# Performance work log

Measured on AMD Instinct MI355X. Metric: run time of the kernel, lower is better.

The kernel has to match this reference:

```python
import jax, jax.numpy as jnp
import numpy as np

N = 20000      # nodes
IN = 256       # in_dim
OUT = 128      # out_dim
S = 8          # num_sect
K = S + 1      # sectors + self branch
EP = 40000     # edges per sector


def setup_inputs() -> dict:
    key = jax.random.key(0)
    ks = jax.random.split(key, 10)
    x = jax.random.normal(ks[0], (N, IN), jnp.float32)
    rows = jax.random.randint(ks[1], (S, EP), 0, N)  # src (adj row)
    cols = jax.random.randint(ks[2], (S, EP), 0, N)  # dst (adj col)
    # degree norms (buffers derived from the graph, as in compute_norm)
    out_deg = np.bincount(np.asarray(rows).ravel(), minlength=N).astype(np.float32)
    in_deg = np.bincount(np.asarray(cols).ravel(), minlength=N).astype(np.float32)
    out_norm = jnp.asarray(np.clip(out_deg, 1.0, None) ** -0.5)[:, None]  # [N,1]
    in_norm = jnp.asarray(np.clip(in_deg, 1.0, None) ** -0.5)[:, None]    # [N,1]
    s = 0.05  # xavier-ish scale
    W_self = jax.random.normal(ks[3], (IN, OUT), jnp.float32) * s
    W_sect = jax.random.normal(ks[4], (S, IN, OUT), jnp.float32) * s
    WC = jax.random.normal(ks[5], (OUT, OUT), jnp.float32) * s
    WD = jax.random.normal(ks[6], (OUT, OUT), jnp.float32) * s
    gate_w = jax.random.normal(ks[7], (2 * K * OUT, 1), jnp.float32) * s
    gate_b = jnp.zeros((1,), jnp.float32)
    return {"x": x, "W_self": W_self, "W_sect": W_sect, "WC": WC, "WD": WD,
            "gate_w": gate_w, "gate_b": gate_b, "out_norm": out_norm,
            "in_norm": in_norm, "rows": rows, "cols": cols}


def reference(x, W_self, W_sect, WC, WD, gate_w, gate_b, out_norm, in_norm, rows, cols):
    n = x.shape[0]
    # --- forward_sector_agg (dropout is identity in eval / drop_rate=0) ---
    z_self = x @ W_self                                    # [N, OUT]
    H = jnp.einsum('ni,sio->sno', x, W_sect) * out_norm    # [S, N, OUT]
    def agg(h, r, c):  # sparse adj @ h : z[src] += h[dst]
        return jax.ops.segment_sum(h[c], r, num_segments=n)
    Z = jax.vmap(agg)(H, rows, cols)                       # [S, N, OUT]
    z = jnp.concatenate([z_self[None], Z], axis=0)         # [K, N, OUT]
    z = jnp.transpose(z, (1, 0, 2)) * in_norm[:, :, None]  # [N, K, OUT]
    # --- heter_sen_interaction ---
    zc = z @ WC                                            # [N, K, D]
    com = jnp.einsum('nkd,njd->nkj', zc, zc)
    ac = jax.nn.softmax(com, axis=2)
    z_com = jnp.einsum('nkj,njd->nkd', ac, zc).reshape(n, -1)
    zd = z @ WD
    sub = zd[:, :, None, :] - zd[:, None, :, :]            # [N, K, K, D]
    ds = jnp.einsum('nkd,nkjd->nkj', zd, sub)
    ad = jax.nn.softmax(ds, axis=2)
    z_dis = jnp.einsum('nkj,nkjd->nkd', ad, sub).reshape(n, -1)
    cat = jnp.concatenate([z_com, z_dis], axis=-1)         # [N, 2*K*D]
    beta = jax.nn.sigmoid(cat @ gate_w + gate_b)           # [N, 1]
    return beta * z_com + (1.0 - beta) * z_dis             # [N, K*D]
```

## Files before the change

### kernel.cpp

```cpp
#include <hip/hip_runtime.h>
#include <math.h>

#define N_NODES 20000
#define IN_DIM  256
#define OUT_DIM 128
#define S_SECT  8
#define K_BR    9
#define NK      (K_BR*OUT_DIM)
#define EP_EDGE 40000
#define N_EDGES (S_SECT*EP_EDGE)
#define N_BINS  (S_SECT*N_NODES)
#define SCAN_BLOCKS 160
#define M_ROWS  (N_NODES*K_BR)
#define ZP      136
#define TP      136

typedef float v4f __attribute__((ext_vector_type(4)));
typedef short v8s __attribute__((ext_vector_type(8)));

__device__ inline unsigned short f2bf(float f) {
  union { float f; unsigned u; } v; v.f = f;
  unsigned r = v.u + 0x7fff + ((v.u >> 16) & 1);
  return (unsigned short)(r >> 16);
}
__device__ inline float bf2f(unsigned short h) {
  union { unsigned u; float f; } v; v.u = ((unsigned)h) << 16;
  return v.f;
}

__global__ __launch_bounds__(256) void k_prep(
    const float* __restrict__ Wself, const float* __restrict__ Wsect,
    const float* __restrict__ WC, const float* __restrict__ WD,
    unsigned short* __restrict__ Wtg, unsigned short* __restrict__ Btg)
{
  const int id = blockIdx.x * 256 + threadIdx.x;
  if (id < NK*IN_DIM) {
    const int j = id >> 8, k = id & 255;
    float w;
    if (j < OUT_DIM) w = Wself[(size_t)k*OUT_DIM + j];
    else {
      const int s = (j - OUT_DIM) >> 7, c = (j - OUT_DIM) & 127;
      w = Wsect[(size_t)s*(IN_DIM*OUT_DIM) + (size_t)k*OUT_DIM + c];
    }
    Wtg[id] = f2bf(w);
  } else {
    const int id2 = id - NK*IN_DIM;
    if (id2 < 256*128) {
      const int n = id2 >> 7, k = id2 & 127;
      const float w = (n < OUT_DIM) ? WC[k*OUT_DIM + n] : WD[k*OUT_DIM + (n - OUT_DIM)];
      Btg[id2] = f2bf(w);
    }
  }
}

__global__ __launch_bounds__(256, 4) void k_gemm_xw_mfma(
    const float* __restrict__ x, const unsigned short* __restrict__ Wtg,
    const float* __restrict__ outn, const float* __restrict__ inn,
    unsigned short* __restrict__ Hbuf, unsigned short* __restrict__ Zbufh)
{
  __shared__ unsigned short Bls[128*ZP];
  const int t = threadIdx.x;
  const int wave = t >> 6, lane = t & 63;
  const int mrow = lane & 15, quad = lane >> 4;
  const int m0 = blockIdx.x * 64 + wave * 16;

  v8s afr[8];
  {
    const int r = m0 + mrow;
    const bool ok = (r < N_NODES);
    const float* src = x + (size_t)r*IN_DIM + quad*8;
    #pragma unroll
    for (int kq = 0; kq < 8; ++kq) {
      float4 a0 = {0.f,0.f,0.f,0.f}, a1 = {0.f,0.f,0.f,0.f};
      if (ok) {
        a0 = *(const float4*)(src + kq*32);
        a1 = *(const float4*)(src + kq*32 + 4);
      }
      v8s f;
      f[0] = (short)f2bf(a0.x); f[1] = (short)f2bf(a0.y);
      f[2] = (short)f2bf(a0.z); f[3] = (short)f2bf(a0.w);
      f[4] = (short)f2bf(a1.x); f[5] = (short)f2bf(a1.y);
      f[6] = (short)f2bf(a1.z); f[7] = (short)f2bf(a1.w);
      afr[kq] = f;
    }
  }

  for (int jj = 0; jj < 3; ++jj) {
    const int jb = blockIdx.y * 3 + jj;

    v4f acc[8];
    #pragma unroll
    for (int jt = 0; jt < 8; ++jt) acc[jt] = (v4f){0.f,0.f,0.f,0.f};

    for (int kh = 0; kh < 2; ++kh) {
      #pragma unroll
      for (int i = 0; i < 8; ++i) {
        const int idx = t + i*256;
        const int row = idx >> 4, c8 = idx & 15;
        *(uint4*)(Bls + row*ZP + c8*8) =
            *(const uint4*)(Wtg + (size_t)(jb*128 + row)*IN_DIM + kh*128 + c8*8);
      }
      __syncthreads();

      #pragma unroll
      for (int kq = 0; kq < 4; ++kq) {
        #pragma unroll
        for (int jt = 0; jt < 8; ++jt) {
          const v8s bf = *(const v8s*)(Bls + (jt*16 + mrow)*ZP + kq*32 + quad*8);
          acc[jt] = __builtin_amdgcn_mfma_f32_16x16x32_bf16(afr[kh*4 + kq], bf, acc[jt], 0, 0, 0);
        }
      }
      __syncthreads();
    }

    if (jb == 0) {
      #pragma unroll
      for (int p = 0; p < 4; ++p) {
        const int R = m0 + quad*4 + p;
        if (R >= N_NODES) continue;
        const float iw = inn[R];
        #pragma unroll
        for (int jt = 0; jt < 8; ++jt)
          Zbufh[(size_t)R*NK + jt*16 + mrow] = f2bf(acc[jt][p] * iw);
      }
    } else {
      const int s = jb - 1;
      #pragma unroll
      for (int p = 0; p < 4; ++p) {
        const int R = m0 + quad*4 + p;
        if (R >= N_NODES) continue;
        const float ow = outn[R];
        #pragma unroll
        for (int jt = 0; jt < 8; ++jt)
          Hbuf[((size_t)s*N_NODES + R)*OUT_DIM + jt*16 + mrow] = f2bf(acc[jt][p] * ow);
      }
    }
  }
}

__global__ __launch_bounds__(256) void k_count(
    const int* __restrict__ rows, int* __restrict__ cnt)
{
  const int id = blockIdx.x * 256 + threadIdx.x;
  if (id >= N_EDGES) return;
  const int s = id / EP_EDGE;
  atomicAdd(&cnt[s * N_NODES + rows[id]], 1);
}

__global__ __launch_bounds__(256) void k_scan1(
    const int* __restrict__ cnt, int* __restrict__ bsum)
{
  __shared__ int sh[256];
  const int t = threadIdx.x;
  const int base = blockIdx.x * 1000;
  int s = 0;
  if (t < 250) {
    const int i = base + t*4;
    s = cnt[i] + cnt[i+1] + cnt[i+2] + cnt[i+3];
  }
  sh[t] = s; __syncthreads();
  for (int off = 128; off > 0; off >>= 1) {
    if (t < off) sh[t] += sh[t + off];
    __syncthreads();
  }
  if (t == 0) bsum[blockIdx.x] = sh[0];
}

__global__ void k_scan2(const int* __restrict__ bsum, int* __restrict__ boff)
{
  if (threadIdx.x == 0) {
    int acc = 0;
    for (int b = 0; b < SCAN_BLOCKS; ++b) { boff[b] = acc; acc += bsum[b]; }
  }
}

__global__ __launch_bounds__(256) void k_scan3(
    const int* __restrict__ cnt, const int* __restrict__ boff,
    int* __restrict__ offs)
{
  __shared__ int sh[256];
  const int t = threadIdx.x;
  const int base = blockIdx.x * 1000;
  int v[4] = {0,0,0,0};
  int mySum = 0;
  if (t < 250) {
    const int i = base + t*4;
    v[0]=cnt[i]; v[1]=cnt[i+1]; v[2]=cnt[i+2]; v[3]=cnt[i+3];
    mySum = v[0]+v[1]+v[2]+v[3];
  }
  sh[t] = mySum; __syncthreads();
  for (int off = 1; off < 256; off <<= 1) {
    int add = (t >= off) ? sh[t - off] : 0;
    __syncthreads();
    sh[t] += add;
    __syncthreads();
  }
  if (t < 250) {
    int excl = boff[blockIdx.x] + sh[t] - mySum;
    const int i = base + t*4;
    offs[i]   = excl;           excl += v[0];
    offs[i+1] = excl;           excl += v[1];
    offs[i+2] = excl;           excl += v[2];
    offs[i+3] = excl;
  }
}

__global__ __launch_bounds__(256) void k_scatter(
    const int* __restrict__ rows, const int* __restrict__ cols,
    const int* __restrict__ offs, int* __restrict__ cur,
    int* __restrict__ eCol)
{
  const int id = blockIdx.x * 256 + threadIdx.x;
  if (id >= N_EDGES) return;
  const int s = id / EP_EDGE;
  const int bin = s * N_NODES + rows[id];
  const int pos = offs[bin] + atomicAdd(&cur[bin], 1);
  eCol[pos] = cols[id];
}

__global__ __launch_bounds__(256) void k_agg_csr(
    const unsigned short* __restrict__ Hbuf, const int* __restrict__ offs,
    const int* __restrict__ cnt, const int* __restrict__ eCol,
    const float* __restrict__ inn, unsigned short* __restrict__ Zbufh)
{
  const long long tid = (long long)blockIdx.x * 256 + threadIdx.x;
  const int group = (int)(tid >> 5);
  if (group >= N_BINS) return;
  const int lane = (int)(tid & 31);
  const int s = group / N_NODES;
  const int r = group - s * N_NODES;
  const int start = offs[group];
  const int n = cnt[group];
  float4 acc = {0.f, 0.f, 0.f, 0.f};
  for (int i = 0; i < n; ++i) {
    const int c = eCol[start + i];
    const uint2 h = *(const uint2*)(Hbuf + ((size_t)s*N_NODES + c)*OUT_DIM + lane*4);
    acc.x += bf2f((unsigned short)h.x);
    acc.y += bf2f((unsigned short)(h.x >> 16));
    acc.z += bf2f((unsigned short)h.y);
    acc.w += bf2f((unsigned short)(h.y >> 16));
  }
  const float w = inn[r];
  uint2 o;
  o.x = (unsigned)f2bf(acc.x * w) | ((unsigned)f2bf(acc.y * w) << 16);
  o.y = (unsigned)f2bf(acc.z * w) | ((unsigned)f2bf(acc.w * w) << 16);
  *(uint2*)(Zbufh + ((size_t)r*K_BR + 1 + s)*OUT_DIM + lane*4) = o;
}

__global__ __launch_bounds__(256, 4) void k_gemm_zcd(
    const unsigned short* __restrict__ Zbufh, const unsigned short* __restrict__ Btg,
    unsigned short* __restrict__ ZCD)
{
  __shared__ unsigned short Bls[128*ZP];
  const int t = threadIdx.x;
  const int wave = t >> 6, lane = t & 63;
  const int m0 = blockIdx.x * 128 + wave * 32;
  const int mrow = lane & 15, quad = lane >> 4;

  v8s afr[2][4];
  #pragma unroll
  for (int rb = 0; rb < 2; ++rb) {
    const int r = m0 + rb*16 + mrow;
    const bool ok = (r < M_ROWS);
    const unsigned short* src = Zbufh + (size_t)r*OUT_DIM + quad*8;
    #pragma unroll
    for (int kq = 0; kq < 4; ++kq) {
      v8s f = {0,0,0,0,0,0,0,0};
      if (ok) f = *(const v8s*)(src + kq*32);
      afr[rb][kq] = f;
    }
  }

  for (int jh = 0; jh < 2; ++jh) {
    #pragma unroll
    for (int i = 0; i < 8; ++i) {
      const int idx = t + i*256;
      const int row = idx >> 4, c8 = idx & 15;
      *(uint4*)(Bls + row*ZP + c8*8) =
          *(const uint4*)(Btg + (size_t)(jh*128 + row)*OUT_DIM + c8*8);
    }
    __syncthreads();

    v4f acc[2][8];
    #pragma unroll
    for (int rb = 0; rb < 2; ++rb)
      #pragma unroll
      for (int j = 0; j < 8; ++j) acc[rb][j] = (v4f){0.f,0.f,0.f,0.f};

    #pragma unroll
    for (int j = 0; j < 8; ++j) {
      const unsigned short* bp = Bls + (j*16 + mrow)*ZP + quad*8;
      #pragma unroll
      for (int kq = 0; kq < 4; ++kq) {
        const v8s bf = *(const v8s*)(bp + kq*32);
        acc[0][j] = __builtin_amdgcn_mfma_f32_16x16x32_bf16(afr[0][kq], bf, acc[0][j], 0, 0, 0);
        acc[1][j] = __builtin_amdgcn_mfma_f32_16x16x32_bf16(afr[1][kq], bf, acc[1][j], 0, 0, 0);
      }
    }

    unsigned short* Z = ZCD + (size_t)jh * N_NODES * NK;
    #pragma unroll
    for (int rb = 0; rb < 2; ++rb)
      #pragma unroll
      for (int p = 0; p < 4; ++p) {
        const int R = m0 + rb*16 + quad*4 + p;
        if (R >= M_ROWS) continue;
        const int node = R / 9, kk = R - node*9;
        const size_t base = (size_t)node*NK + kk*OUT_DIM;
        #pragma unroll
        for (int j = 0; j < 8; ++j)
          Z[base + j*16 + mrow] = f2bf(acc[rb][j][p]);
      }
    __syncthreads();
  }
}

__global__ __launch_bounds__(256) void k_interact5(
    const unsigned short* __restrict__ ZCD,
    const float* __restrict__ gw, const float* __restrict__ gb,
    float* __restrict__ out)
{
  __shared__ unsigned short tls[8][2][9*TP];
  __shared__ float graw[8][2][K_BR][10];
  __shared__ float gs[8][2][K_BR][10];
  const int t  = threadIdx.x;
  const int wv = t >> 6, lane = t & 63;
  const int n0 = blockIdx.x * 8;

  {
    const int r = lane & 15, quad = lane >> 4;
    #pragma unroll
    for (int q = 0; q < 4; ++q) {
      const int node = wv*2 + (q >> 1), mat = q & 1;
      const unsigned short* src = ZCD + (size_t)mat*N_NODES*NK
                                  + (size_t)(n0+node)*NK + (size_t)r*OUT_DIM + quad*8;
      v8s frag[4];
      #pragma unroll
      for (int kq = 0; kq < 4; ++kq) {
        v8s f = {0,0,0,0,0,0,0,0};
        if (r < K_BR) f = *(const v8s*)(src + kq*32);
        frag[kq] = f;
      }
      if (r < K_BR) {
        #pragma unroll
        for (int kq = 0; kq < 4; ++kq)
          *(v8s*)&tls[node][mat][r*TP + kq*32 + quad*8] = frag[kq];
      }
      v4f acc = {0.f,0.f,0.f,0.f};
      #pragma unroll
      for (int kq = 0; kq < 4; ++kq)
        acc = __builtin_amdgcn_mfma_f32_16x16x32_bf16(frag[kq], frag[kq], acc, 0, 0, 0);
      if (r < K_BR) {
        #pragma unroll
        for (int p = 0; p < 4; ++p) {
          const int m = quad*4 + p;
          if (m < K_BR) graw[node][mat][m][r] = acc[p];
        }
      }
    }
  }
  __syncthreads();

  if (lane < 36) {
    const int nn2  = (lane >= 18) ? 1 : 0;
    const int node = wv*2 + nn2;
    const int rem  = lane - nn2*18;
    const int mat  = (rem >= 9) ? 1 : 0;
    const int k    = rem - mat*9;
    float v[9];
    if (mat == 0) {
      #pragma unroll
      for (int j = 0; j < 9; ++j) v[j] = graw[node][0][k][j];
    } else {
      const float gkk = graw[node][1][k][k];
      #pragma unroll
      for (int j = 0; j < 9; ++j) v[j] = gkk - graw[node][1][k][j];
    }
    float m = v[0];
    #pragma unroll
    for (int j = 1; j < 9; ++j) m = fmaxf(m, v[j]);
    float sum = 0.f;
    #pragma unroll
    for (int j = 0; j < 9; ++j) { v[j] = expf(v[j] - m); sum += v[j]; }
    const float inv = 1.f / sum;
    #pragma unroll
    for (int j = 0; j < 9; ++j) gs[node][mat][k][j] = v[j] * inv;
  }
  __syncthreads();

  const float gbv = gb[0];
  float gwc[2][9], gwd[2][9];
  #pragma unroll
  for (int dd = 0; dd < 2; ++dd) {
    const int d = lane + dd*64;
    #pragma unroll
    for (int j = 0; j < 9; ++j) {
      gwc[dd][j] = gw[j*OUT_DIM + d];
      gwd[dd][j] = gw[NK + j*OUT_DIM + d];
    }
  }

  for (int nn = 0; nn < 2; ++nn) {
    const int node = wv*2 + nn;
    float zcj[2][9], zdj[2][9];
    #pragma unroll
    for (int dd = 0; dd < 2; ++dd) {
      const int d = lane + dd*64;
      #pragma unroll
      for (int j = 0; j < 9; ++j) {
        zcj[dd][j] = bf2f(tls[node][0][j*TP + d]);
        zdj[dd][j] = bf2f(tls[node][1][j*TP + d]);
      }
    }
    float zcomK[2][9], zdisK[2][9];
    float gp = 0.f;
    #pragma unroll
    for (int k = 0; k < 9; ++k) {
      #pragma unroll
      for (int dd = 0; dd < 2; ++dd) {
        float zc = 0.f, ad = 0.f;
        #pragma unroll
        for (int j = 0; j < 9; ++j) {
          zc += gs[node][0][k][j] * zcj[dd][j];
          ad += gs[node][1][k][j] * zdj[dd][j];
        }
        zcomK[dd][k] = zc;
        zdisK[dd][k] = zdj[dd][k] - ad;
        gp += zc * gwc[dd][k] + zdisK[dd][k] * gwd[dd][k];
      }
    }
    #pragma unroll
    for (int off = 32; off > 0; off >>= 1) gp += __shfl_xor(gp, off, 64);
    const float beta = 1.f / (1.f + expf(-(gp + gbv)));
    #pragma unroll
    for (int k = 0; k < 9; ++k) {
      #pragma unroll
      for (int dd = 0; dd < 2; ++dd) {
        const int d = lane + dd*64;
        out[(size_t)(n0+node)*NK + k*OUT_DIM + d] =
            beta*zcomK[dd][k] + (1.f-beta)*zdisK[dd][k];
      }
    }
  }
}

extern "C" void kernel_launch(void* const* d_in, const int* in_sizes, int n_in,
                              void* d_out, int out_size, void* d_ws, size_t ws_size,
                              hipStream_t stream)
{
  const float* x     = (const float*)d_in[0];
  const float* Wself = (const float*)d_in[1];
  const float* Wsect = (const float*)d_in[2];
  const float* WC    = (const float*)d_in[3];
  const float* WD    = (const float*)d_in[4];
  const float* gw    = (const float*)d_in[5];
  const float* gb    = (const float*)d_in[6];
  const float* outn  = (const float*)d_in[7];
  const float* inn   = (const float*)d_in[8];
  const int*   rows  = (const int*)d_in[9];
  const int*   cols  = (const int*)d_in[10];
  float* out = (float*)d_out;

  char* p = (char*)d_ws;
  unsigned short* Hbuf  = (unsigned short*)p; p += (size_t)S_SECT*N_NODES*OUT_DIM*2;
  unsigned short* Zbufh = (unsigned short*)p; p += (size_t)M_ROWS*OUT_DIM*2;
  unsigned short* ZCD   = (unsigned short*)p; p += (size_t)2*N_NODES*NK*2;
  int* cnt    = (int*)p;                      p += (size_t)N_BINS*4;
  int* offs   = (int*)p;                      p += (size_t)N_BINS*4;
  int* cur    = (int*)p;                      p += (size_t)N_BINS*4;
  int* bsum   = (int*)p;                      p += 256*4;
  int* boff   = (int*)p;                      p += 256*4;
  int* eCol   = (int*)p;                      p += (size_t)N_EDGES*4;
  unsigned short* Btg = (unsigned short*)p;   p += 256*128*2;
  unsigned short* Wtg = (unsigned short*)p;   p += (size_t)NK*IN_DIM*2;

  hipMemsetAsync(cnt, 0, (size_t)N_BINS*4, stream);
  hipMemsetAsync(cur, 0, (size_t)N_BINS*4, stream);

  k_prep<<<(NK*IN_DIM + 256*128 + 255)/256, 256, 0, stream>>>(Wself, Wsect, WC, WD, Wtg, Btg);

  dim3 gA((N_NODES + 63)/64, 3);
  k_gemm_xw_mfma<<<gA, 256, 0, stream>>>(x, Wtg, outn, inn, Hbuf, Zbufh);

  const int eb = (N_EDGES + 255)/256;
  k_count  <<<eb, 256, 0, stream>>>(rows, cnt);
  k_scan1  <<<SCAN_BLOCKS, 256, 0, stream>>>(cnt, bsum);
  k_scan2  <<<1, 64, 0, stream>>>(bsum, boff);
  k_scan3  <<<SCAN_BLOCKS, 256, 0, stream>>>(cnt, boff, offs);
  k_scatter<<<eb, 256, 0, stream>>>(rows, cols, offs, cur, eCol);

  const int aggBlocks = (N_BINS*32 + 255)/256;
  k_agg_csr<<<aggBlocks, 256, 0, stream>>>(Hbuf, offs, cnt, eCol, inn, Zbufh);

  k_gemm_zcd<<<(M_ROWS + 127)/128, 256, 0, stream>>>(Zbufh, Btg, ZCD);

  k_interact5<<<N_NODES/8, 256, 0, stream>>>(ZCD, gw, gb, out);
}
```

Baseline: 316.6 us.

## Fuse ZC/ZD projection GEMM into interaction kernel, keeping results in LDS

The separate bf16 GEMM that produced the ZC/ZD projections into a global ZCD buffer is merged into the per-node interaction kernel. Each wave now computes the projections for its two nodes (18 rows padded to 32) and writes them straight into the shared-memory tiles that the interaction stage already used. This removes a large global write and read-back of the intermediate projections, plus one kernel launch. In exchange, part of the MFMA work on padded rows is wasted, the weight matrix is reloaded into LDS by every block in 64-row chunks, and the larger shared-memory footprint lowers occupancy.

```diff
diff --git a/kernel.cpp b/kernel.cpp
--- a/kernel.cpp
+++ b/kernel.cpp
@@ -247,22 +247,27 @@
   *(uint2*)(Zbufh + ((size_t)r*K_BR + 1 + s)*OUT_DIM + lane*4) = o;
 }
 
-__global__ __launch_bounds__(256, 4) void k_gemm_zcd(
+__global__ __launch_bounds__(256, 2) void k_zcd_interact(
     const unsigned short* __restrict__ Zbufh, const unsigned short* __restrict__ Btg,
-    unsigned short* __restrict__ ZCD)
-{
-  __shared__ unsigned short Bls[128*ZP];
+    const float* __restrict__ gw, const float* __restrict__ gb,
+    float* __restrict__ out)
+{
+  __shared__ unsigned short Bls[64*ZP];
+  __shared__ unsigned short tls[8][2][9*TP];
+  __shared__ float graw[8][2][K_BR][10];
+  __shared__ float gs[8][2][K_BR][10];
   const int t = threadIdx.x;
-  const int wave = t >> 6, lane = t & 63;
-  const int m0 = blockIdx.x * 128 + wave * 32;
+  const int wv = t >> 6, lane = t & 63;
   const int mrow = lane & 15, quad = lane >> 4;
+  const int n0 = blockIdx.x * 8;
+  const int rowbase = (n0 + 2*wv)*9;
 
   v8s afr[2][4];
   #pragma unroll
   for (int rb = 0; rb < 2; ++rb) {
-    const int r = m0 + rb*16 + mrow;
-    const bool ok = (r < M_ROWS);
-    const unsigned short* src = Zbufh + (size_t)r*OUT_DIM + quad*8;
+    const int rloc = rb*16 + mrow;
+    const bool ok = (rloc < 18);
+    const unsigned short* src = Zbufh + (size_t)(rowbase + rloc)*OUT_DIM + quad*8;
     #pragma unroll
     for (int kq = 0; kq < 4; ++kq) {
       v8s f = {0,0,0,0,0,0,0,0};
@@ -272,68 +277,55 @@
   }
 
   for (int jh = 0; jh < 2; ++jh) {
-    #pragma unroll
-    for (int i = 0; i < 8; ++i) {
-      const int idx = t + i*256;
-      const int row = idx >> 4, c8 = idx & 15;
-      *(uint4*)(Bls + row*ZP + c8*8) =
-          *(const uint4*)(Btg + (size_t)(jh*128 + row)*OUT_DIM + c8*8);
-    }
-    __syncthreads();
-
     v4f acc[2][8];
     #pragma unroll
     for (int rb = 0; rb < 2; ++rb)
       #pragma unroll
       for (int j = 0; j < 8; ++j) acc[rb][j] = (v4f){0.f,0.f,0.f,0.f};
 
-    #pragma unroll
-    for (int j = 0; j < 8; ++j) {
-      const unsigned short* bp = Bls + (j*16 + mrow)*ZP + quad*8;
-      #pragma unroll
-      for (int kq = 0; kq < 4; ++kq) {
-        const v8s bf = *(const v8s*)(bp + kq*32);
-        acc[0][j] = __builtin_amdgcn_mfma_f32_16x16x32_bf16(afr[0][kq], bf, acc[0][j], 0, 0, 0);
-        acc[1][j] = __builtin_amdgcn_mfma_f32_16x16x32_bf16(afr[1][kq], bf, acc[1][j], 0, 0, 0);
-      }
-    }
-
-    unsigned short* Z = ZCD + (size_t)jh * N_NODES * NK;
+    for (int sub = 0; sub < 2; ++sub) {
+      #pragma unroll
+      for (int i = 0; i < 4; ++i) {
+        const int idx = t + i*256;
+        const int row = idx >> 4, c8 = idx & 15;
+        *(uint4*)(Bls + row*ZP + c8*8) =
+            *(const uint4*)(Btg + (size_t)(jh*128 + sub*64 + row)*OUT_DIM + c8*8);
+      }
+      __syncthreads();
+      #pragma unroll
+      for (int jl = 0; jl < 4; ++jl) {
+        const unsigned short* bp = Bls + (jl*16 + mrow)*ZP + quad*8;
+        #pragma unroll
+        for (int kq = 0; kq < 4; ++kq) {
+          const v8s bf = *(const v8s*)(bp + kq*32);
+          acc[0][sub*4+jl] = __builtin_amdgcn_mfma_f32_16x16x32_bf16(afr[0][kq], bf, acc[0][sub*4+jl], 0, 0, 0);
+          acc[1][sub*4+jl] = __builtin_amdgcn_mfma_f32_16x16x32_bf16(afr[1][kq], bf, acc[1][sub*4+jl], 0, 0, 0);
+        }
+      }
+      __syncthreads();
+    }
+
     #pragma unroll
     for (int rb = 0; rb < 2; ++rb)
       #pragma unroll
       for (int p = 0; p < 4; ++p) {
-        const int R = m0 + rb*16 + quad*4 + p;
-        if (R >= M_ROWS) continue;
-        const int node = R / 9, kk = R - node*9;
-        const size_t base = (size_t)node*NK + kk*OUT_DIM;
-        #pragma unroll
-        for (int j = 0; j < 8; ++j)
-          Z[base + j*16 + mrow] = f2bf(acc[rb][j][p]);
-      }
-    __syncthreads();
-  }
-}
-
-__global__ __launch_bounds__(256) void k_interact5(
-    const unsigned short* __restrict__ ZCD,
-    const float* __restrict__ gw, const float* __restrict__ gb,
-    float* __restrict__ out)
-{
-  __shared__ unsigned short tls[8][2][9*TP];
-  __shared__ float graw[8][2][K_BR][10];
-  __shared__ float gs[8][2][K_BR][10];
-  const int t  = threadIdx.x;
-  const int wv = t >> 6, lane = t & 63;
-  const int n0 = blockIdx.x * 8;
+        const int R = rb*16 + quad*4 + p;
+        if (R >= 18) continue;
+        const int nn = (R >= 9) ? 1 : 0;
+        const int kk = R - nn*9;
+        unsigned short* dst = &tls[wv*2 + nn][jh][kk*TP + mrow];
+        #pragma unroll
+        for (int jj = 0; jj < 8; ++jj)
+          dst[jj*16] = f2bf(acc[rb][jj][p]);
+      }
+  }
 
   {
-    const int r = lane & 15, quad = lane >> 4;
+    const int r = lane & 15;
     #pragma unroll
     for (int q = 0; q < 4; ++q) {
       const int node = wv*2 + (q >> 1), mat = q & 1;
-      const unsigned short* src = ZCD + (size_t)mat*N_NODES*NK
-                                  + (size_t)(n0+node)*NK + (size_t)r*OUT_DIM + quad*8;
+      const unsigned short* src = &tls[node][mat][r*TP + quad*8];
       v8s frag[4];
       #pragma unroll
       for (int kq = 0; kq < 4; ++kq) {
@@ -341,11 +333,6 @@
         if (r < K_BR) f = *(const v8s*)(src + kq*32);
         frag[kq] = f;
       }
-      if (r < K_BR) {
-        #pragma unroll
-        for (int kq = 0; kq < 4; ++kq)
-          *(v8s*)&tls[node][mat][r*TP + kq*32 + quad*8] = frag[kq];
-      }
       v4f acc = {0.f,0.f,0.f,0.f};
       #pragma unroll
       for (int kq = 0; kq < 4; ++kq)
@@ -359,7 +346,6 @@
       }
     }
   }
-  __syncthreads();
 
   if (lane < 36) {
     const int nn2  = (lane >= 18) ? 1 : 0;
@@ -386,7 +372,6 @@
     #pragma unroll
     for (int j = 0; j < 9; ++j) gs[node][mat][k][j] = v[j] * inv;
   }
-  __syncthreads();
 
   const float gbv = gb[0];
   float gwc[2][9], gwd[2][9];
@@ -464,7 +449,6 @@
   char* p = (char*)d_ws;
   unsigned short* Hbuf  = (unsigned short*)p; p += (size_t)S_SECT*N_NODES*OUT_DIM*2;
   unsigned short* Zbufh = (unsigned short*)p; p += (size_t)M_ROWS*OUT_DIM*2;
-  unsigned short* ZCD   = (unsigned short*)p; p += (size_t)2*N_NODES*NK*2;
   int* cnt    = (int*)p;                      p += (size_t)N_BINS*4;
   int* offs   = (int*)p;                      p += (size_t)N_BINS*4;
   int* cur    = (int*)p;                      p += (size_t)N_BINS*4;
@@ -492,7 +476,5 @@
   const int aggBlocks = (N_BINS*32 + 255)/256;
   k_agg_csr<<<aggBlocks, 256, 0, stream>>>(Hbuf, offs, cnt, eCol, inn, Zbufh);
 
-  k_gemm_zcd<<<(M_ROWS + 127)/128, 256, 0, stream>>>(Zbufh, Btg, ZCD);
-
-  k_interact5<<<N_NODES/8, 256, 0, stream>>>(ZCD, gw, gb, out);
-}
+  k_zcd_interact<<<N_NODES/8, 256, 0, stream>>>(Zbufh, Btg, gw, gb, out);
+}
```

Result: faster. 298.4 us (-5.7%).
